# Kernel optimization log

Hardware: AMD Instinct MI355X
Metric: run time of the kernel (lower is better)

## Reference

```python
import jax, jax.numpy as jnp
import numpy as np

N, IN_DIM, HID, HEADS, OUT = 4096, 512, 256, 2, 40
LN_EPS = 1e-5


def setup_inputs() -> dict:
    key = jax.random.key(0)
    ks = jax.random.split(key, 12)
    s_in = 1.0 / np.sqrt(IN_DIM)
    s_o = 1.0 / np.sqrt(2 * HID)
    adj = jax.random.randint(ks[0], (HEADS, N, N), 0, 2).astype(jnp.float32)
    h = jax.random.normal(ks[1], (N, IN_DIM), dtype=jnp.float32)
    Wq = jax.random.uniform(ks[2], (HEADS, IN_DIM, HID), minval=-s_in, maxval=s_in)
    bq = jax.random.uniform(ks[3], (HEADS, HID), minval=-s_in, maxval=s_in)
    Wk = jax.random.uniform(ks[4], (HEADS, IN_DIM, HID), minval=-s_in, maxval=s_in)
    bk = jax.random.uniform(ks[5], (HEADS, HID), minval=-s_in, maxval=s_in)
    Wv = jax.random.uniform(ks[6], (HEADS, IN_DIM, HID), minval=-s_in, maxval=s_in)
    bv = jax.random.uniform(ks[7], (HEADS, HID), minval=-s_in, maxval=s_in)
    Wo = jax.random.uniform(ks[8], (2 * HID, IN_DIM), minval=-s_o, maxval=s_o)
    bo = jax.random.uniform(ks[9], (IN_DIM,), minval=-s_o, maxval=s_o)
    gamma = jnp.ones((IN_DIM,), jnp.float32)
    beta = jnp.zeros((IN_DIM,), jnp.float32)
    Wp = jax.random.uniform(ks[10], (IN_DIM, OUT), minval=-s_in, maxval=s_in)
    bp = jax.random.uniform(ks[11], (OUT,), minval=-s_in, maxval=s_in)
    return dict(adj=adj, h=h, Wq=Wq, bq=bq, Wk=Wk, bk=bk, Wv=Wv, bv=bv,
                Wo=Wo, bo=bo, gamma=gamma, beta=beta, Wp=Wp, bp=bp)


def reference(adj, h, Wq, bq, Wk, bk, Wv, bv, Wo, bo, gamma, beta, Wp, bp):
    # Per-head projections, vectorized over the head axis. [H, N, D]
    Q = jnp.einsum('ni,hid->hnd', h, Wq) + bq[:, None, :]
    K = jnp.einsum('ni,hid->hnd', h, Wk) + bk[:, None, :]
    V = jnp.einsum('ni,hid->hnd', h, Wv) + bv[:, None, :]
    # Dense QK^T, elementwise-multiplied (not -inf masked) by per-head adjacency.
    scores = jnp.einsum('hnd,hmd->hnm', Q, K) * adj          # [H, N, N]
    attn = jax.nn.softmax(scores, axis=-1)
    X = jnp.einsum('hnm,hmd->hnd', attn, V)                  # [H, N, D]
    # cat([X0, X1], dim=1) -> [N, H*D]
    X_final = jnp.transpose(X, (1, 0, 2)).reshape(N, HEADS * HID)
    z = X_final @ Wo + bo                                    # [N, IN_DIM]
    mu = jnp.mean(z, axis=-1, keepdims=True)
    var = jnp.var(z, axis=-1, keepdims=True)
    M = (z - mu) * jax.lax.rsqrt(var + LN_EPS) * gamma + beta
    return jax.nn.softmax(M @ Wp + bp, axis=1)               # [N, OUT]
```

## Files before the change

kernel.cpp:

```cpp
#include <hip/hip_runtime.h>
#include <hip/hip_bf16.h>

#define N_TOK 4096
#define D_IN  512
#define D_HID 256
#define N_OUT 40

typedef _Float16 half8 __attribute__((ext_vector_type(8)));
typedef _Float16 half4 __attribute__((ext_vector_type(4)));
typedef float    f32x4 __attribute__((ext_vector_type(4)));

__device__ __forceinline__ void async_copy16(const _Float16* g, _Float16* l) {
  __builtin_amdgcn_global_load_lds(
      (const __attribute__((address_space(1))) unsigned int*)(g),
      (__attribute__((address_space(3))) unsigned int*)(l), 16, 0, 0);
}

__device__ __forceinline__ void transpose_tile(const float* __restrict__ src, int in_ncols,
                                               _Float16* __restrict__ dst, int out_ncols,
                                               int i0, int d0, float* lds )
{
  int tid = threadIdx.x;
  int l15 = tid & 15, l4 = tid >> 4;
#pragma unroll
  for (int p = 0; p < 4; p++) {
    int ii = p * 16 + l4;
    float4 x = *(const float4*)(src + (size_t)(i0 + ii) * in_ncols + d0 + l15 * 4);
    lds[(l15 * 4 + 0) * 65 + ii] = x.x;
    lds[(l15 * 4 + 1) * 65 + ii] = x.y;
    lds[(l15 * 4 + 2) * 65 + ii] = x.z;
    lds[(l15 * 4 + 3) * 65 + ii] = x.w;
  }
  __syncthreads();
  int dd = tid >> 2, chunk = tid & 3;
  half8 o0, o1;
#pragma unroll
  for (int j = 0; j < 8; j++) o0[j] = (_Float16)lds[dd * 65 + chunk * 16 + j];
#pragma unroll
  for (int j = 0; j < 8; j++) o1[j] = (_Float16)lds[dd * 65 + chunk * 16 + 8 + j];
  *(half8*)(dst + (size_t)(d0 + dd) * out_ncols + i0 + chunk * 16) = o0;
  *(half8*)(dst + (size_t)(d0 + dd) * out_ncols + i0 + chunk * 16 + 8) = o1;
}

__global__ void prep_kernel(const float* __restrict__ h, const float* __restrict__ Wq,
                            const float* __restrict__ Wk, const float* __restrict__ Wv,
                            const float* __restrict__ Wo, const float* __restrict__ Wp,
                            _Float16* __restrict__ h16, _Float16* __restrict__ Wqt,
                            _Float16* __restrict__ Wkt, _Float16* __restrict__ Wvt,
                            _Float16* __restrict__ Wot, _Float16* __restrict__ Wpt)
{
  __shared__ float lds[64 * 65];
  int b = blockIdx.x, tid = threadIdx.x;
  if (b < 1024) {
    int base = b * 2048 + tid * 8;
    float4 x0 = *(const float4*)(h + base);
    float4 x1 = *(const float4*)(h + base + 4);
    half8 o;
    o[0]=(_Float16)x0.x; o[1]=(_Float16)x0.y; o[2]=(_Float16)x0.z; o[3]=(_Float16)x0.w;
    o[4]=(_Float16)x1.x; o[5]=(_Float16)x1.y; o[6]=(_Float16)x1.z; o[7]=(_Float16)x1.w;
    *(half8*)(h16 + base) = o;
  } else if (b < 1216) {
    int t = b - 1024;
    int mat = t >> 5;
    int m = mat >> 1, head = mat & 1;
    const float* W = (m==0 ? Wq : (m==1 ? Wk : Wv)) + head * (D_IN * D_HID);
    _Float16* Wt   = (m==0 ? Wqt : (m==1 ? Wkt : Wvt)) + head * (D_IN * D_HID);
    int tt = t & 31;
    int i0 = (tt >> 2) * 64, d0 = (tt & 3) * 64;
    transpose_tile(W, D_HID, Wt, D_IN, i0, d0, lds);
  } else if (b < 1280) {
    int t = b - 1216;
    int i0 = (t >> 3) * 64, d0 = (t & 7) * 64;
    transpose_tile(Wo, D_IN, Wot, D_IN, i0, d0, lds);
  } else {
    int blk = b - 1280;
    int idx = blk * 1024 + tid * 4;
    int j = idx >> 9, i = idx & 511;
    half4 o;
#pragma unroll
    for (int u = 0; u < 4; u++)
      o[u] = (j < N_OUT) ? (_Float16)Wp[(i + u) * N_OUT + j] : (_Float16)0.f;
    *(half4*)(Wpt + j * D_IN + i) = o;
  }
}

__global__ __launch_bounds__(256, 2) void proj_kernel(
    const _Float16* __restrict__ h16, const _Float16* __restrict__ W6 ,
    const _Float16* __restrict__ Wvt,
    const float* __restrict__ bq, const float* __restrict__ bk,
    const float* __restrict__ bv,
    _Float16* __restrict__ Q16, _Float16* __restrict__ K16,
    _Float16* __restrict__ VT16)
{
  __shared__ __align__(16) _Float16 Atile[128 * 64];
  __shared__ __align__(16) _Float16 Btile[128 * 64];

  int b = blockIdx.x;
  int tid = threadIdx.x, w = tid >> 6, lane = tid & 63, quad = lane >> 4, cL = lane & 15;
  int wr = w >> 1, wc = w & 1;

  const _Float16 *Asrc, *Bsrc;
  int isV;
  int m0 = 0, n0 = 0, head = 0, mh = 0;
  if (b < 256) {
    isV = 0;
    m0 = (b >> 3) * 128;
    int ct = b & 7;
    mh = ct >> 1;
    n0 = (ct & 1) * 128;
    Asrc = h16 + (size_t)m0 * D_IN;
    Bsrc = W6 + (size_t)(ct * 128) * D_IN;
  } else {
    isV = 1;
    int t = b - 256;
    head = t >> 6;
    int tt = t & 63;
    m0 = (tt >> 5) * 128;
    n0 = (tt & 31) * 128;
    Asrc = Wvt + (size_t)head * (D_HID * D_IN) + (size_t)m0 * D_IN;
    Bsrc = h16 + (size_t)n0 * D_IN;
  }

  const f32x4 z4 = {0.f, 0.f, 0.f, 0.f};
  f32x4 acc[4][4];
#pragma unroll
  for (int i = 0; i < 4; i++)
#pragma unroll
    for (int j = 0; j < 4; j++) acc[i][j] = z4;

  int r8 = lane >> 3, chs = (lane & 7) ^ r8;

  for (int kc = 0; kc < 8; kc++) {
    __syncthreads();
#pragma unroll
    for (int g = 0; g < 4; g++) {
      int row = (w * 4 + g) * 8 + r8;
      async_copy16(Asrc + (size_t)row * D_IN + kc * 64 + chs * 8, Atile + (w * 4 + g) * 512);
      async_copy16(Bsrc + (size_t)row * D_IN + kc * 64 + chs * 8, Btile + (w * 4 + g) * 512);
    }
    __syncthreads();
#pragma unroll
    for (int kk = 0; kk < 2; kk++) {
      int ch = ((kk * 4 + quad) ^ (cL & 7)) * 8;
      half8 a[4], bf[4];
#pragma unroll
      for (int mt = 0; mt < 4; mt++)
        a[mt] = *(const half8*)(Atile + (wr * 64 + mt * 16 + cL) * 64 + ch);
#pragma unroll
      for (int nt = 0; nt < 4; nt++)
        bf[nt] = *(const half8*)(Btile + (wc * 64 + nt * 16 + cL) * 64 + ch);
#pragma unroll
      for (int mt = 0; mt < 4; mt++)
#pragma unroll
        for (int nt = 0; nt < 4; nt++)
          acc[mt][nt] = __builtin_amdgcn_mfma_f32_16x16x32_f16(a[mt], bf[nt], acc[mt][nt], 0, 0, 0);
    }
  }

  if (!isV) {
    _Float16* Out = (mh < 2 ? Q16 + (size_t)mh * (N_TOK * D_HID)
                            : K16 + (size_t)(mh - 2) * (N_TOK * D_HID));
    const float* bias = (mh < 2 ? bq + mh * D_HID : bk + (mh - 2) * D_HID);
#pragma unroll
    for (int mt = 0; mt < 4; mt++) {
      int row = m0 + wr * 64 + mt * 16 + quad * 4;
#pragma unroll
      for (int nt = 0; nt < 4; nt++) {
        int colg = n0 + wc * 64 + nt * 16 + cL;
        float bb = bias[colg];
#pragma unroll
        for (int reg = 0; reg < 4; reg++)
          Out[(size_t)(row + reg) * D_HID + colg] = (_Float16)(acc[mt][nt][reg] + bb);
      }
    }
  } else {
    _Float16* VTh = VT16 + (size_t)head * (N_TOK * D_HID);
    const float* bvh = bv + head * D_HID;
#pragma unroll
    for (int mt = 0; mt < 4; mt++) {
      int d0r = m0 + wr * 64 + mt * 16 + quad * 4;
      float bvv[4];
#pragma unroll
      for (int reg = 0; reg < 4; reg++) bvv[reg] = bvh[d0r + reg];
#pragma unroll
      for (int nt = 0; nt < 4; nt++) {
        int tok = n0 + wc * 64 + nt * 16 + cL;
#pragma unroll
        for (int reg = 0; reg < 4; reg++)
          VTh[(size_t)(d0r + reg) * N_TOK + tok] = (_Float16)(acc[mt][nt][reg] + bvv[reg]);
      }
    }
  }
}

__global__ __launch_bounds__(256, 2) void attn_kernel(
    const float* __restrict__ adj, const _Float16* __restrict__ Q16,
    const _Float16* __restrict__ K16, const _Float16* __restrict__ VT16,
    _Float16* __restrict__ Opart, float* __restrict__ Mpart, float* __restrict__ Lpart)
{
  __shared__ __align__(16) _Float16 Ktile[64 * 256];
  __shared__ __align__(16) _Float16 VTtile[256 * 64];
  __shared__ __align__(16) _Float16 Pbuf[4 * 16 * 72];

  int b = blockIdx.x;
  int head = (b >> 2) & 1;
  int gs = b & 3;
  int q0 = (b >> 3) * 64;

  int tid = threadIdx.x;
  int w = tid >> 6, lane = tid & 63, quad = lane >> 4, cL = lane & 15;

  const _Float16* Qh = Q16 + head * (N_TOK * D_HID);
  const _Float16* Kh = K16 + head * (N_TOK * D_HID);
  const _Float16* Vh = VT16 + head * (N_TOK * D_HID);
  const float* adjh = adj + (size_t)head * N_TOK * N_TOK;

  int qrow = q0 + w * 16;
  int nstart = gs * 1024;
  const f32x4 z4 = {0.f, 0.f, 0.f, 0.f};

  half8 qf[8];
#pragma unroll
  for (int t = 0; t < 8; t++)
    qf[t] = *(const half8*)(Qh + (qrow + cL) * D_HID + t * 32 + quad * 8);

  f32x4 acc[16];
#pragma unroll
  for (int i = 0; i < 16; i++) acc[i] = z4;
  float m_i[4] = {-1e30f, -1e30f, -1e30f, -1e30f};
  float l_i[4] = {0.f, 0.f, 0.f, 0.f};

  _Float16* pb = Pbuf + w * (16 * 72);

  const float* adjR[4];
#pragma unroll
  for (int reg = 0; reg < 4; reg++)
    adjR[reg] = adjh + (size_t)(qrow + quad * 4 + reg) * N_TOK + nstart + cL;

  int l5 = lane >> 5, l31 = lane & 31;
  int l3 = lane >> 3, l7 = lane & 7;

  for (int it = 0; it < 16; ++it) {
    int n0 = nstart + it * 64;

    __syncthreads();

#pragma unroll
    for (int i = 0; i < 8; i++) {
      int g = w * 8 + i;
      int rK = 2 * g + l5;
      int cK = l31 ^ (rK & 7);
      async_copy16(Kh + (size_t)(n0 + rK) * D_HID + cK * 8, Ktile + g * 512);
      int rV = g * 8 + l3;
      int cV = l7 ^ (rV & 7);
      async_copy16(Vh + (size_t)rV * N_TOK + n0 + cV * 8, VTtile + g * 512);
    }
    float av[4][4];
#pragma unroll
    for (int reg = 0; reg < 4; reg++)
#pragma unroll
      for (int ct = 0; ct < 4; ct++)
        av[reg][ct] = __builtin_nontemporal_load(adjR[reg] + it * 64 + ct * 16);

    __syncthreads();

    f32x4 s[4];
#pragma unroll
    for (int ct = 0; ct < 4; ct++) s[ct] = z4;
#pragma unroll
    for (int t = 0; t < 8; t++) {
#pragma unroll
      for (int ct = 0; ct < 4; ct++) {
        int rK = ct * 16 + cL;
        int ck = (t * 4 + quad) ^ (rK & 7);
        half8 kf = *(const half8*)(Ktile + rK * 256 + ck * 8);
        s[ct] = __builtin_amdgcn_mfma_f32_16x16x32_f16(qf[t], kf, s[ct], 0, 0, 0);
      }
    }

    float alpha[4];
#pragma unroll
    for (int reg = 0; reg < 4; reg++) {
#pragma unroll
      for (int ct = 0; ct < 4; ct++) s[ct][reg] *= av[reg][ct];
      float mx = fmaxf(fmaxf(s[0][reg], s[1][reg]), fmaxf(s[2][reg], s[3][reg]));
#pragma unroll
      for (int msk = 1; msk < 16; msk <<= 1) mx = fmaxf(mx, __shfl_xor(mx, msk, 16));
      float mnew = fmaxf(m_i[reg], mx);
      alpha[reg] = __expf(m_i[reg] - mnew);
      m_i[reg] = mnew;
      float rs = 0.f;
#pragma unroll
      for (int ct = 0; ct < 4; ct++) {
        float p = __expf(s[ct][reg] - mnew);
        s[ct][reg] = p;
        rs += p;
      }
#pragma unroll
      for (int msk = 1; msk < 16; msk <<= 1) rs += __shfl_xor(rs, msk, 16);
      l_i[reg] = l_i[reg] * alpha[reg] + rs;
    }

#pragma unroll
    for (int reg = 0; reg < 4; reg++)
#pragma unroll
      for (int ct = 0; ct < 4; ct++)
        pb[(quad * 4 + reg) * 72 + ct * 16 + cL] = (_Float16)s[ct][reg];

#pragma unroll
    for (int dt = 0; dt < 16; dt++)
#pragma unroll
      for (int reg = 0; reg < 4; reg++)
        acc[dt][reg] *= alpha[reg];

    half8 pf0 = *(const half8*)(pb + cL * 72 + quad * 8);
    half8 pf1 = *(const half8*)(pb + cL * 72 + 32 + quad * 8);
#pragma unroll
    for (int dt = 0; dt < 16; dt++) {
      int rV = dt * 16 + cL;
      int c0 = (quad) ^ (rV & 7);
      int c1 = (4 + quad) ^ (rV & 7);
      half8 v0 = *(const half8*)(VTtile + rV * 64 + c0 * 8);
      half8 v1 = *(const half8*)(VTtile + rV * 64 + c1 * 8);
      acc[dt] = __builtin_amdgcn_mfma_f32_16x16x32_f16(pf0, v0, acc[dt], 0, 0, 0);
      acc[dt] = __builtin_amdgcn_mfma_f32_16x16x32_f16(pf1, v1, acc[dt], 0, 0, 0);
    }
  }

  int prow = (head * 4 + gs) * N_TOK + qrow + quad * 4;
#pragma unroll
  for (int reg = 0; reg < 4; reg++) {
    int row = prow + reg;
#pragma unroll
    for (int dt = 0; dt < 16; dt++)
      Opart[(size_t)row * D_HID + dt * 16 + cL] = (_Float16)acc[dt][reg];
    if (cL == 0) { Mpart[row] = m_i[reg]; Lpart[row] = l_i[reg]; }
  }
}

__global__ void merge_kernel(const _Float16* __restrict__ Opart,
                             const float* __restrict__ Mpart,
                             const float* __restrict__ Lpart,
                             _Float16* __restrict__ Xf)
{
  int t = blockIdx.x * 256 + threadIdx.x;
  int dg = (t & 63) << 2;
  int n = (t >> 6) & (N_TOK - 1);
  int head = t >> 18;
  int idx[4];
  float m[4], l[4];
  float mm = -1e30f;
#pragma unroll
  for (int s = 0; s < 4; s++) {
    idx[s] = (head * 4 + s) * N_TOK + n;
    m[s] = Mpart[idx[s]];
    l[s] = Lpart[idx[s]];
    mm = fmaxf(mm, m[s]);
  }
  float f[4], L = 0.f;
#pragma unroll
  for (int s = 0; s < 4; s++) { f[s] = __expf(m[s] - mm); L += f[s] * l[s]; }
  float rl = 1.0f / L;
  float o[4] = {0.f, 0.f, 0.f, 0.f};
#pragma unroll
  for (int s = 0; s < 4; s++) {
    half4 os = *(const half4*)(Opart + (size_t)idx[s] * D_HID + dg);
#pragma unroll
    for (int u = 0; u < 4; u++) o[u] += (float)os[u] * f[s];
  }
  half4 res;
#pragma unroll
  for (int u = 0; u < 4; u++) res[u] = (_Float16)(o[u] * rl);
  *(half4*)(Xf + (size_t)n * D_IN + head * D_HID + dg) = res;
}

__global__ __launch_bounds__(256, 1) void final_kernel(
    const _Float16* __restrict__ Xf, const _Float16* __restrict__ Wot,
    const _Float16* __restrict__ Wpt, const float* __restrict__ bo,
    const float* __restrict__ gamma, const float* __restrict__ beta,
    const float* __restrict__ bp, float* __restrict__ out)
{
  __shared__ __align__(16) _Float16 Btile[512 * 64];
  __shared__ __align__(16) _Float16 Mlds[16 * 520];
  __shared__ float outs[16 * 48];
  __shared__ float lnsum[4][16], lnsq[4][16];
  __shared__ float smx[16], srl[16];

  int rowbase = blockIdx.x * 16;
  int tid = threadIdx.x, w = tid >> 6, lane = tid & 63, quad = lane >> 4, cL = lane & 15;
  const f32x4 z4 = {0.f, 0.f, 0.f, 0.f};

  half8 af[16];
#pragma unroll
  for (int t = 0; t < 16; t++)
    af[t] = *(const half8*)(Xf + (rowbase + cL) * D_IN + t * 32 + quad * 8);

  f32x4 acc[8];
#pragma unroll
  for (int i = 0; i < 8; i++) acc[i] = z4;

  int r8 = lane >> 3, chs = (lane & 7) ^ r8;

  for (int kc = 0; kc < 8; kc++) {
    __syncthreads();
#pragma unroll
    for (int g = 0; g < 16; g++) {
      int row = (w * 16 + g) * 8 + r8;
      async_copy16(Wot + (size_t)row * D_IN + kc * 64 + chs * 8, Btile + (w * 16 + g) * 512);
    }
    __syncthreads();
#pragma unroll
    for (int kk = 0; kk < 2; kk++) {
      int ch = ((kk * 4 + quad) ^ (cL & 7)) * 8;
      half8 a = af[kc * 2 + kk];
      half8 bf[8];
#pragma unroll
      for (int nt = 0; nt < 8; nt++)
        bf[nt] = *(const half8*)(Btile + (w * 128 + nt * 16 + cL) * 64 + ch);
#pragma unroll
      for (int nt = 0; nt < 8; nt++)
        acc[nt] = __builtin_amdgcn_mfma_f32_16x16x32_f16(a, bf[nt], acc[nt], 0, 0, 0);
    }
  }

  float sum[4] = {0, 0, 0, 0}, sq[4] = {0, 0, 0, 0};
#pragma unroll
  for (int nt = 0; nt < 8; nt++) {
    int col = w * 128 + nt * 16 + cL;
    float bb = bo[col];
#pragma unroll
    for (int reg = 0; reg < 4; reg++) {
      float z = acc[nt][reg] + bb;
      acc[nt][reg] = z;
      sum[reg] += z;
      sq[reg] += z * z;
    }
  }
#pragma unroll
  for (int reg = 0; reg < 4; reg++) {
#pragma unroll
    for (int msk = 1; msk < 16; msk <<= 1) {
      sum[reg] += __shfl_xor(sum[reg], msk, 16);
      sq[reg]  += __shfl_xor(sq[reg], msk, 16);
    }
  }
  if (cL == 0) {
#pragma unroll
    for (int reg = 0; reg < 4; reg++) {
      lnsum[w][quad * 4 + reg] = sum[reg];
      lnsq[w][quad * 4 + reg]  = sq[reg];
    }
  }
  __syncthreads();
  float mean[4], rstd[4];
#pragma unroll
  for (int reg = 0; reg < 4; reg++) {
    int row = quad * 4 + reg;
    float s  = lnsum[0][row] + lnsum[1][row] + lnsum[2][row] + lnsum[3][row];
    float s2 = lnsq[0][row]  + lnsq[1][row]  + lnsq[2][row]  + lnsq[3][row];
    float mu = s * (1.0f / 512.0f);
    float var = s2 * (1.0f / 512.0f) - mu * mu;
    mean[reg] = mu;
    rstd[reg] = rsqrtf(var + 1e-5f);
  }
#pragma unroll
  for (int nt = 0; nt < 8; nt++) {
    int col = w * 128 + nt * 16 + cL;
    float g = gamma[col], be = beta[col];
#pragma unroll
    for (int reg = 0; reg < 4; reg++) {
      float mval = (acc[nt][reg] - mean[reg]) * rstd[reg] * g + be;
      Mlds[(quad * 4 + reg) * 520 + col] = (_Float16)mval;
    }
  }
  __syncthreads();
  if (w < 3) {
    int jt = w;
    f32x4 a2 = z4;
#pragma unroll
    for (int t = 0; t < 16; t++) {
      half8 am = *(const half8*)(Mlds + cL * 520 + t * 32 + quad * 8);
      half8 bm = *(const half8*)(Wpt + (jt * 16 + cL) * D_IN + t * 32 + quad * 8);
      a2 = __builtin_amdgcn_mfma_f32_16x16x32_f16(am, bm, a2, 0, 0, 0);
    }
    int col = jt * 16 + cL;
    float bpv = (col < N_OUT) ? bp[col] : 0.0f;
#pragma unroll
    for (int reg = 0; reg < 4; reg++)
      outs[(quad * 4 + reg) * 48 + col] = a2[reg] + bpv;
  }
  __syncthreads();
  if (tid < 16) {
    int row = tid;
    float mx = -1e30f;
    for (int j = 0; j < N_OUT; j++) mx = fmaxf(mx, outs[row * 48 + j]);
    float ssum = 0.f;
    for (int j = 0; j < N_OUT; j++) ssum += __expf(outs[row * 48 + j] - mx);
    smx[row] = mx;
    srl[row] = 1.0f / ssum;
  }
  __syncthreads();
#pragma unroll
  for (int i = 0; i < 3; i++) {
    int lin = tid + 256 * i;
    if (lin < 16 * N_OUT) {
      int row = lin / N_OUT, col = lin % N_OUT;
      out[(size_t)(rowbase + row) * N_OUT + col] =
          __expf(outs[row * 48 + col] - smx[row]) * srl[row];
    }
  }
}

#define OFF_WOT   0u
#define OFF_WPT   524288u
#define OFF_Q16   573440u
#define OFF_K16   4767744u
#define OFF_VT16  8962048u
#define OFF_MP    13156352u
#define OFF_LP    13287424u
#define OFF_XF    13418496u
#define OFF_OP    17612800u
#define OFF_H16   17612800u
#define OFF_WQT   21807104u
#define OFF_WKT   22331392u
#define OFF_WVT   22855680u

extern "C" void kernel_launch(void* const* d_in, const int* in_sizes, int n_in,
                              void* d_out, int out_size, void* d_ws, size_t ws_size,
                              hipStream_t stream)
{
  const float* adj   = (const float*)d_in[0];
  const float* h     = (const float*)d_in[1];
  const float* Wq    = (const float*)d_in[2];
  const float* bq    = (const float*)d_in[3];
  const float* Wk    = (const float*)d_in[4];
  const float* bk    = (const float*)d_in[5];
  const float* Wv    = (const float*)d_in[6];
  const float* bv    = (const float*)d_in[7];
  const float* Wo    = (const float*)d_in[8];
  const float* bo    = (const float*)d_in[9];
  const float* gamma = (const float*)d_in[10];
  const float* beta  = (const float*)d_in[11];
  const float* Wp    = (const float*)d_in[12];
  const float* bp    = (const float*)d_in[13];
  float* out = (float*)d_out;
  char* ws = (char*)d_ws;

  _Float16* h16   = (_Float16*)(ws + OFF_H16);
  _Float16* Wqt   = (_Float16*)(ws + OFF_WQT);
  _Float16* Wkt   = (_Float16*)(ws + OFF_WKT);
  _Float16* Wvt   = (_Float16*)(ws + OFF_WVT);
  _Float16* Wot   = (_Float16*)(ws + OFF_WOT);
  _Float16* Wpt   = (_Float16*)(ws + OFF_WPT);
  _Float16* Q16   = (_Float16*)(ws + OFF_Q16);
  _Float16* K16   = (_Float16*)(ws + OFF_K16);
  _Float16* VT16  = (_Float16*)(ws + OFF_VT16);
  _Float16* Opart = (_Float16*)(ws + OFF_OP);
  float*    Mpart = (float*)(ws + OFF_MP);
  float*    Lpart = (float*)(ws + OFF_LP);
  _Float16* Xf    = (_Float16*)(ws + OFF_XF);

  prep_kernel<<<1304, 256, 0, stream>>>(h, Wq, Wk, Wv, Wo, Wp,
                                        h16, Wqt, Wkt, Wvt, Wot, Wpt);
  proj_kernel<<<384, 256, 0, stream>>>(h16, Wqt, Wvt, bq, bk, bv,
                                       Q16, K16, VT16);
  attn_kernel<<<512, 256, 0, stream>>>(adj, Q16, K16, VT16, Opart, Mpart, Lpart);
  merge_kernel<<<2048, 256, 0, stream>>>(Opart, Mpart, Lpart, Xf);
  final_kernel<<<256, 256, 0, stream>>>(Xf, Wot, Wpt, bo, gamma, beta, bp, out);
}
```

Measured before the change: 297.9 us.

## Fuse all stages into one cooperative persistent kernel with grid syncs

```diff
diff --git a/kernel.cpp b/kernel.cpp
--- a/kernel.cpp
+++ b/kernel.cpp
@@ -1,5 +1,5 @@
 #include <hip/hip_runtime.h>
-#include <hip/hip_bf16.h>
+#include <hip/hip_cooperative_groups.h>
 
 #define N_TOK 4096
 #define D_IN  512
@@ -16,500 +16,11 @@
       (__attribute__((address_space(3))) unsigned int*)(l), 16, 0, 0);
 }
 
-__device__ __forceinline__ void transpose_tile(const float* __restrict__ src, int in_ncols,
-                                               _Float16* __restrict__ dst, int out_ncols,
-                                               int i0, int d0, float* lds )
-{
-  int tid = threadIdx.x;
-  int l15 = tid & 15, l4 = tid >> 4;
-#pragma unroll
-  for (int p = 0; p < 4; p++) {
-    int ii = p * 16 + l4;
-    float4 x = *(const float4*)(src + (size_t)(i0 + ii) * in_ncols + d0 + l15 * 4);
-    lds[(l15 * 4 + 0) * 65 + ii] = x.x;
-    lds[(l15 * 4 + 1) * 65 + ii] = x.y;
-    lds[(l15 * 4 + 2) * 65 + ii] = x.z;
-    lds[(l15 * 4 + 3) * 65 + ii] = x.w;
-  }
-  __syncthreads();
-  int dd = tid >> 2, chunk = tid & 3;
-  half8 o0, o1;
-#pragma unroll
-  for (int j = 0; j < 8; j++) o0[j] = (_Float16)lds[dd * 65 + chunk * 16 + j];
-#pragma unroll
-  for (int j = 0; j < 8; j++) o1[j] = (_Float16)lds[dd * 65 + chunk * 16 + 8 + j];
-  *(half8*)(dst + (size_t)(d0 + dd) * out_ncols + i0 + chunk * 16) = o0;
-  *(half8*)(dst + (size_t)(d0 + dd) * out_ncols + i0 + chunk * 16 + 8) = o1;
-}
-
-__global__ void prep_kernel(const float* __restrict__ h, const float* __restrict__ Wq,
-                            const float* __restrict__ Wk, const float* __restrict__ Wv,
-                            const float* __restrict__ Wo, const float* __restrict__ Wp,
-                            _Float16* __restrict__ h16, _Float16* __restrict__ Wqt,
-                            _Float16* __restrict__ Wkt, _Float16* __restrict__ Wvt,
-                            _Float16* __restrict__ Wot, _Float16* __restrict__ Wpt)
-{
-  __shared__ float lds[64 * 65];
-  int b = blockIdx.x, tid = threadIdx.x;
-  if (b < 1024) {
-    int base = b * 2048 + tid * 8;
-    float4 x0 = *(const float4*)(h + base);
-    float4 x1 = *(const float4*)(h + base + 4);
-    half8 o;
-    o[0]=(_Float16)x0.x; o[1]=(_Float16)x0.y; o[2]=(_Float16)x0.z; o[3]=(_Float16)x0.w;
-    o[4]=(_Float16)x1.x; o[5]=(_Float16)x1.y; o[6]=(_Float16)x1.z; o[7]=(_Float16)x1.w;
-    *(half8*)(h16 + base) = o;
-  } else if (b < 1216) {
-    int t = b - 1024;
-    int mat = t >> 5;
-    int m = mat >> 1, head = mat & 1;
-    const float* W = (m==0 ? Wq : (m==1 ? Wk : Wv)) + head * (D_IN * D_HID);
-    _Float16* Wt   = (m==0 ? Wqt : (m==1 ? Wkt : Wvt)) + head * (D_IN * D_HID);
-    int tt = t & 31;
-    int i0 = (tt >> 2) * 64, d0 = (tt & 3) * 64;
-    transpose_tile(W, D_HID, Wt, D_IN, i0, d0, lds);
-  } else if (b < 1280) {
-    int t = b - 1216;
-    int i0 = (t >> 3) * 64, d0 = (t & 7) * 64;
-    transpose_tile(Wo, D_IN, Wot, D_IN, i0, d0, lds);
-  } else {
-    int blk = b - 1280;
-    int idx = blk * 1024 + tid * 4;
-    int j = idx >> 9, i = idx & 511;
-    half4 o;
-#pragma unroll
-    for (int u = 0; u < 4; u++)
-      o[u] = (j < N_OUT) ? (_Float16)Wp[(i + u) * N_OUT + j] : (_Float16)0.f;
-    *(half4*)(Wpt + j * D_IN + i) = o;
-  }
-}
-
-__global__ __launch_bounds__(256, 2) void proj_kernel(
-    const _Float16* __restrict__ h16, const _Float16* __restrict__ W6 ,
-    const _Float16* __restrict__ Wvt,
-    const float* __restrict__ bq, const float* __restrict__ bk,
-    const float* __restrict__ bv,
-    _Float16* __restrict__ Q16, _Float16* __restrict__ K16,
-    _Float16* __restrict__ VT16)
-{
-  __shared__ __align__(16) _Float16 Atile[128 * 64];
-  __shared__ __align__(16) _Float16 Btile[128 * 64];
-
-  int b = blockIdx.x;
-  int tid = threadIdx.x, w = tid >> 6, lane = tid & 63, quad = lane >> 4, cL = lane & 15;
-  int wr = w >> 1, wc = w & 1;
-
-  const _Float16 *Asrc, *Bsrc;
-  int isV;
-  int m0 = 0, n0 = 0, head = 0, mh = 0;
-  if (b < 256) {
-    isV = 0;
-    m0 = (b >> 3) * 128;
-    int ct = b & 7;
-    mh = ct >> 1;
-    n0 = (ct & 1) * 128;
-    Asrc = h16 + (size_t)m0 * D_IN;
-    Bsrc = W6 + (size_t)(ct * 128) * D_IN;
-  } else {
-    isV = 1;
-    int t = b - 256;
-    head = t >> 6;
-    int tt = t & 63;
-    m0 = (tt >> 5) * 128;
-    n0 = (tt & 31) * 128;
-    Asrc = Wvt + (size_t)head * (D_HID * D_IN) + (size_t)m0 * D_IN;
-    Bsrc = h16 + (size_t)n0 * D_IN;
-  }
-
-  const f32x4 z4 = {0.f, 0.f, 0.f, 0.f};
-  f32x4 acc[4][4];
-#pragma unroll
-  for (int i = 0; i < 4; i++)
-#pragma unroll
-    for (int j = 0; j < 4; j++) acc[i][j] = z4;
-
-  int r8 = lane >> 3, chs = (lane & 7) ^ r8;
-
-  for (int kc = 0; kc < 8; kc++) {
-    __syncthreads();
-#pragma unroll
-    for (int g = 0; g < 4; g++) {
-      int row = (w * 4 + g) * 8 + r8;
-      async_copy16(Asrc + (size_t)row * D_IN + kc * 64 + chs * 8, Atile + (w * 4 + g) * 512);
-      async_copy16(Bsrc + (size_t)row * D_IN + kc * 64 + chs * 8, Btile + (w * 4 + g) * 512);
-    }
-    __syncthreads();
-#pragma unroll
-    for (int kk = 0; kk < 2; kk++) {
-      int ch = ((kk * 4 + quad) ^ (cL & 7)) * 8;
-      half8 a[4], bf[4];
-#pragma unroll
-      for (int mt = 0; mt < 4; mt++)
-        a[mt] = *(const half8*)(Atile + (wr * 64 + mt * 16 + cL) * 64 + ch);
-#pragma unroll
-      for (int nt = 0; nt < 4; nt++)
-        bf[nt] = *(const half8*)(Btile + (wc * 64 + nt * 16 + cL) * 64 + ch);
-#pragma unroll
-      for (int mt = 0; mt < 4; mt++)
-#pragma unroll
-        for (int nt = 0; nt < 4; nt++)
-          acc[mt][nt] = __builtin_amdgcn_mfma_f32_16x16x32_f16(a[mt], bf[nt], acc[mt][nt], 0, 0, 0);
-    }
-  }
-
-  if (!isV) {
-    _Float16* Out = (mh < 2 ? Q16 + (size_t)mh * (N_TOK * D_HID)
-                            : K16 + (size_t)(mh - 2) * (N_TOK * D_HID));
-    const float* bias = (mh < 2 ? bq + mh * D_HID : bk + (mh - 2) * D_HID);
-#pragma unroll
-    for (int mt = 0; mt < 4; mt++) {
-      int row = m0 + wr * 64 + mt * 16 + quad * 4;
-#pragma unroll
-      for (int nt = 0; nt < 4; nt++) {
-        int colg = n0 + wc * 64 + nt * 16 + cL;
-        float bb = bias[colg];
-#pragma unroll
-        for (int reg = 0; reg < 4; reg++)
-          Out[(size_t)(row + reg) * D_HID + colg] = (_Float16)(acc[mt][nt][reg] + bb);
-      }
-    }
-  } else {
-    _Float16* VTh = VT16 + (size_t)head * (N_TOK * D_HID);
-    const float* bvh = bv + head * D_HID;
-#pragma unroll
-    for (int mt = 0; mt < 4; mt++) {
-      int d0r = m0 + wr * 64 + mt * 16 + quad * 4;
-      float bvv[4];
-#pragma unroll
-      for (int reg = 0; reg < 4; reg++) bvv[reg] = bvh[d0r + reg];
-#pragma unroll
-      for (int nt = 0; nt < 4; nt++) {
-        int tok = n0 + wc * 64 + nt * 16 + cL;
-#pragma unroll
-        for (int reg = 0; reg < 4; reg++)
-          VTh[(size_t)(d0r + reg) * N_TOK + tok] = (_Float16)(acc[mt][nt][reg] + bvv[reg]);
-      }
-    }
-  }
-}
-
-__global__ __launch_bounds__(256, 2) void attn_kernel(
-    const float* __restrict__ adj, const _Float16* __restrict__ Q16,
-    const _Float16* __restrict__ K16, const _Float16* __restrict__ VT16,
-    _Float16* __restrict__ Opart, float* __restrict__ Mpart, float* __restrict__ Lpart)
-{
-  __shared__ __align__(16) _Float16 Ktile[64 * 256];
-  __shared__ __align__(16) _Float16 VTtile[256 * 64];
-  __shared__ __align__(16) _Float16 Pbuf[4 * 16 * 72];
-
-  int b = blockIdx.x;
-  int head = (b >> 2) & 1;
-  int gs = b & 3;
-  int q0 = (b >> 3) * 64;
-
-  int tid = threadIdx.x;
-  int w = tid >> 6, lane = tid & 63, quad = lane >> 4, cL = lane & 15;
-
-  const _Float16* Qh = Q16 + head * (N_TOK * D_HID);
-  const _Float16* Kh = K16 + head * (N_TOK * D_HID);
-  const _Float16* Vh = VT16 + head * (N_TOK * D_HID);
-  const float* adjh = adj + (size_t)head * N_TOK * N_TOK;
-
-  int qrow = q0 + w * 16;
-  int nstart = gs * 1024;
-  const f32x4 z4 = {0.f, 0.f, 0.f, 0.f};
-
-  half8 qf[8];
-#pragma unroll
-  for (int t = 0; t < 8; t++)
-    qf[t] = *(const half8*)(Qh + (qrow + cL) * D_HID + t * 32 + quad * 8);
-
-  f32x4 acc[16];
-#pragma unroll
-  for (int i = 0; i < 16; i++) acc[i] = z4;
-  float m_i[4] = {-1e30f, -1e30f, -1e30f, -1e30f};
-  float l_i[4] = {0.f, 0.f, 0.f, 0.f};
-
-  _Float16* pb = Pbuf + w * (16 * 72);
-
-  const float* adjR[4];
-#pragma unroll
-  for (int reg = 0; reg < 4; reg++)
-    adjR[reg] = adjh + (size_t)(qrow + quad * 4 + reg) * N_TOK + nstart + cL;
-
-  int l5 = lane >> 5, l31 = lane & 31;
-  int l3 = lane >> 3, l7 = lane & 7;
-
-  for (int it = 0; it < 16; ++it) {
-    int n0 = nstart + it * 64;
-
-    __syncthreads();
-
-#pragma unroll
-    for (int i = 0; i < 8; i++) {
-      int g = w * 8 + i;
-      int rK = 2 * g + l5;
-      int cK = l31 ^ (rK & 7);
-      async_copy16(Kh + (size_t)(n0 + rK) * D_HID + cK * 8, Ktile + g * 512);
-      int rV = g * 8 + l3;
-      int cV = l7 ^ (rV & 7);
-      async_copy16(Vh + (size_t)rV * N_TOK + n0 + cV * 8, VTtile + g * 512);
-    }
-    float av[4][4];
-#pragma unroll
-    for (int reg = 0; reg < 4; reg++)
-#pragma unroll
-      for (int ct = 0; ct < 4; ct++)
-        av[reg][ct] = __builtin_nontemporal_load(adjR[reg] + it * 64 + ct * 16);
-
-    __syncthreads();
-
-    f32x4 s[4];
-#pragma unroll
-    for (int ct = 0; ct < 4; ct++) s[ct] = z4;
-#pragma unroll
-    for (int t = 0; t < 8; t++) {
-#pragma unroll
-      for (int ct = 0; ct < 4; ct++) {
-        int rK = ct * 16 + cL;
-        int ck = (t * 4 + quad) ^ (rK & 7);
-        half8 kf = *(const half8*)(Ktile + rK * 256 + ck * 8);
-        s[ct] = __builtin_amdgcn_mfma_f32_16x16x32_f16(qf[t], kf, s[ct], 0, 0, 0);
-      }
-    }
-
-    float alpha[4];
-#pragma unroll
-    for (int reg = 0; reg < 4; reg++) {
-#pragma unroll
-      for (int ct = 0; ct < 4; ct++) s[ct][reg] *= av[reg][ct];
-      float mx = fmaxf(fmaxf(s[0][reg], s[1][reg]), fmaxf(s[2][reg], s[3][reg]));
-#pragma unroll
-      for (int msk = 1; msk < 16; msk <<= 1) mx = fmaxf(mx, __shfl_xor(mx, msk, 16));
-      float mnew = fmaxf(m_i[reg], mx);
-      alpha[reg] = __expf(m_i[reg] - mnew);
-      m_i[reg] = mnew;
-      float rs = 0.f;
-#pragma unroll
-      for (int ct = 0; ct < 4; ct++) {
-        float p = __expf(s[ct][reg] - mnew);
-        s[ct][reg] = p;
-        rs += p;
-      }
-#pragma unroll
-      for (int msk = 1; msk < 16; msk <<= 1) rs += __shfl_xor(rs, msk, 16);
-      l_i[reg] = l_i[reg] * alpha[reg] + rs;
-    }
-
-#pragma unroll
-    for (int reg = 0; reg < 4; reg++)
-#pragma unroll
-      for (int ct = 0; ct < 4; ct++)
-        pb[(quad * 4 + reg) * 72 + ct * 16 + cL] = (_Float16)s[ct][reg];
-
-#pragma unroll
-    for (int dt = 0; dt < 16; dt++)
-#pragma unroll
-      for (int reg = 0; reg < 4; reg++)
-        acc[dt][reg] *= alpha[reg];
-
-    half8 pf0 = *(const half8*)(pb + cL * 72 + quad * 8);
-    half8 pf1 = *(const half8*)(pb + cL * 72 + 32 + quad * 8);
-#pragma unroll
-    for (int dt = 0; dt < 16; dt++) {
-      int rV = dt * 16 + cL;
-      int c0 = (quad) ^ (rV & 7);
-      int c1 = (4 + quad) ^ (rV & 7);
-      half8 v0 = *(const half8*)(VTtile + rV * 64 + c0 * 8);
-      half8 v1 = *(const half8*)(VTtile + rV * 64 + c1 * 8);
-      acc[dt] = __builtin_amdgcn_mfma_f32_16x16x32_f16(pf0, v0, acc[dt], 0, 0, 0);
-      acc[dt] = __builtin_amdgcn_mfma_f32_16x16x32_f16(pf1, v1, acc[dt], 0, 0, 0);
-    }
-  }
-
-  int prow = (head * 4 + gs) * N_TOK + qrow + quad * 4;
-#pragma unroll
-  for (int reg = 0; reg < 4; reg++) {
-    int row = prow + reg;
-#pragma unroll
-    for (int dt = 0; dt < 16; dt++)
-      Opart[(size_t)row * D_HID + dt * 16 + cL] = (_Float16)acc[dt][reg];
-    if (cL == 0) { Mpart[row] = m_i[reg]; Lpart[row] = l_i[reg]; }
-  }
-}
-
-__global__ void merge_kernel(const _Float16* __restrict__ Opart,
-                             const float* __restrict__ Mpart,
-                             const float* __restrict__ Lpart,
-                             _Float16* __restrict__ Xf)
-{
-  int t = blockIdx.x * 256 + threadIdx.x;
-  int dg = (t & 63) << 2;
-  int n = (t >> 6) & (N_TOK - 1);
-  int head = t >> 18;
-  int idx[4];
-  float m[4], l[4];
-  float mm = -1e30f;
-#pragma unroll
-  for (int s = 0; s < 4; s++) {
-    idx[s] = (head * 4 + s) * N_TOK + n;
-    m[s] = Mpart[idx[s]];
-    l[s] = Lpart[idx[s]];
-    mm = fmaxf(mm, m[s]);
-  }
-  float f[4], L = 0.f;
-#pragma unroll
-  for (int s = 0; s < 4; s++) { f[s] = __expf(m[s] - mm); L += f[s] * l[s]; }
-  float rl = 1.0f / L;
-  float o[4] = {0.f, 0.f, 0.f, 0.f};
-#pragma unroll
-  for (int s = 0; s < 4; s++) {
-    half4 os = *(const half4*)(Opart + (size_t)idx[s] * D_HID + dg);
-#pragma unroll
-    for (int u = 0; u < 4; u++) o[u] += (float)os[u] * f[s];
-  }
-  half4 res;
-#pragma unroll
-  for (int u = 0; u < 4; u++) res[u] = (_Float16)(o[u] * rl);
-  *(half4*)(Xf + (size_t)n * D_IN + head * D_HID + dg) = res;
-}
-
-__global__ __launch_bounds__(256, 1) void final_kernel(
-    const _Float16* __restrict__ Xf, const _Float16* __restrict__ Wot,
-    const _Float16* __restrict__ Wpt, const float* __restrict__ bo,
-    const float* __restrict__ gamma, const float* __restrict__ beta,
-    const float* __restrict__ bp, float* __restrict__ out)
-{
-  __shared__ __align__(16) _Float16 Btile[512 * 64];
-  __shared__ __align__(16) _Float16 Mlds[16 * 520];
-  __shared__ float outs[16 * 48];
-  __shared__ float lnsum[4][16], lnsq[4][16];
-  __shared__ float smx[16], srl[16];
-
-  int rowbase = blockIdx.x * 16;
-  int tid = threadIdx.x, w = tid >> 6, lane = tid & 63, quad = lane >> 4, cL = lane & 15;
-  const f32x4 z4 = {0.f, 0.f, 0.f, 0.f};
-
-  half8 af[16];
-#pragma unroll
-  for (int t = 0; t < 16; t++)
-    af[t] = *(const half8*)(Xf + (rowbase + cL) * D_IN + t * 32 + quad * 8);
-
-  f32x4 acc[8];
-#pragma unroll
-  for (int i = 0; i < 8; i++) acc[i] = z4;
-
-  int r8 = lane >> 3, chs = (lane & 7) ^ r8;
-
-  for (int kc = 0; kc < 8; kc++) {
-    __syncthreads();
-#pragma unroll
-    for (int g = 0; g < 16; g++) {
-      int row = (w * 16 + g) * 8 + r8;
-      async_copy16(Wot + (size_t)row * D_IN + kc * 64 + chs * 8, Btile + (w * 16 + g) * 512);
-    }
-    __syncthreads();
-#pragma unroll
-    for (int kk = 0; kk < 2; kk++) {
-      int ch = ((kk * 4 + quad) ^ (cL & 7)) * 8;
-      half8 a = af[kc * 2 + kk];
-      half8 bf[8];
-#pragma unroll
-      for (int nt = 0; nt < 8; nt++)
-        bf[nt] = *(const half8*)(Btile + (w * 128 + nt * 16 + cL) * 64 + ch);
-#pragma unroll
-      for (int nt = 0; nt < 8; nt++)
-        acc[nt] = __builtin_amdgcn_mfma_f32_16x16x32_f16(a, bf[nt], acc[nt], 0, 0, 0);
-    }
-  }
-
-  float sum[4] = {0, 0, 0, 0}, sq[4] = {0, 0, 0, 0};
-#pragma unroll
-  for (int nt = 0; nt < 8; nt++) {
-    int col = w * 128 + nt * 16 + cL;
-    float bb = bo[col];
-#pragma unroll
-    for (int reg = 0; reg < 4; reg++) {
-      float z = acc[nt][reg] + bb;
-      acc[nt][reg] = z;
-      sum[reg] += z;
-      sq[reg] += z * z;
-    }
-  }
-#pragma unroll
-  for (int reg = 0; reg < 4; reg++) {
-#pragma unroll
-    for (int msk = 1; msk < 16; msk <<= 1) {
-      sum[reg] += __shfl_xor(sum[reg], msk, 16);
-      sq[reg]  += __shfl_xor(sq[reg], msk, 16);
-    }
-  }
-  if (cL == 0) {
-#pragma unroll
-    for (int reg = 0; reg < 4; reg++) {
-      lnsum[w][quad * 4 + reg] = sum[reg];
-      lnsq[w][quad * 4 + reg]  = sq[reg];
-    }
-  }
-  __syncthreads();
-  float mean[4], rstd[4];
-#pragma unroll
-  for (int reg = 0; reg < 4; reg++) {
-    int row = quad * 4 + reg;
-    float s  = lnsum[0][row] + lnsum[1][row] + lnsum[2][row] + lnsum[3][row];
-    float s2 = lnsq[0][row]  + lnsq[1][row]  + lnsq[2][row]  + lnsq[3][row];
-    float mu = s * (1.0f / 512.0f);
-    float var = s2 * (1.0f / 512.0f) - mu * mu;
-    mean[reg] = mu;
-    rstd[reg] = rsqrtf(var + 1e-5f);
-  }
-#pragma unroll
-  for (int nt = 0; nt < 8; nt++) {
-    int col = w * 128 + nt * 16 + cL;
-    float g = gamma[col], be = beta[col];
-#pragma unroll
-    for (int reg = 0; reg < 4; reg++) {
-      float mval = (acc[nt][reg] - mean[reg]) * rstd[reg] * g + be;
-      Mlds[(quad * 4 + reg) * 520 + col] = (_Float16)mval;
-    }
-  }
-  __syncthreads();
-  if (w < 3) {
-    int jt = w;
-    f32x4 a2 = z4;
-#pragma unroll
-    for (int t = 0; t < 16; t++) {
-      half8 am = *(const half8*)(Mlds + cL * 520 + t * 32 + quad * 8);
-      half8 bm = *(const half8*)(Wpt + (jt * 16 + cL) * D_IN + t * 32 + quad * 8);
-      a2 = __builtin_amdgcn_mfma_f32_16x16x32_f16(am, bm, a2, 0, 0, 0);
-    }
-    int col = jt * 16 + cL;
-    float bpv = (col < N_OUT) ? bp[col] : 0.0f;
-#pragma unroll
-    for (int reg = 0; reg < 4; reg++)
-      outs[(quad * 4 + reg) * 48 + col] = a2[reg] + bpv;
-  }
-  __syncthreads();
-  if (tid < 16) {
-    int row = tid;
-    float mx = -1e30f;
-    for (int j = 0; j < N_OUT; j++) mx = fmaxf(mx, outs[row * 48 + j]);
-    float ssum = 0.f;
-    for (int j = 0; j < N_OUT; j++) ssum += __expf(outs[row * 48 + j] - mx);
-    smx[row] = mx;
-    srl[row] = 1.0f / ssum;
-  }
-  __syncthreads();
-#pragma unroll
-  for (int i = 0; i < 3; i++) {
-    int lin = tid + 256 * i;
-    if (lin < 16 * N_OUT) {
-      int row = lin / N_OUT, col = lin % N_OUT;
-      out[(size_t)(rowbase + row) * N_OUT + col] =
-          __expf(outs[row * 48 + col] - smx[row]) * srl[row];
-    }
-  }
-}
+struct Params {
+  const float *adj, *h, *Wq, *bq, *Wk, *bk, *Wv, *bv, *Wo, *bo, *gamma, *beta, *Wp, *bp;
+  float* out;
+  char* ws;
+};
 
 #define OFF_WOT   0u
 #define OFF_WPT   524288u
@@ -518,53 +29,528 @@
 #define OFF_VT16  8962048u
 #define OFF_MP    13156352u
 #define OFF_LP    13287424u
-#define OFF_XF    13418496u
 #define OFF_OP    17612800u
 #define OFF_H16   17612800u
 #define OFF_WQT   21807104u
 #define OFF_WKT   22331392u
 #define OFF_WVT   22855680u
 
+__global__ __launch_bounds__(256, 2) void fused_kernel(Params P, int phase)
+{
+  __shared__ __align__(16) char smem[74752];
+  const int bid = blockIdx.x, tid = threadIdx.x;
+  const int w = tid >> 6, lane = tid & 63, quad = lane >> 4, cL = lane & 15;
+  const f32x4 z4 = {0.f, 0.f, 0.f, 0.f};
+
+  char* ws = P.ws;
+  _Float16* Wot  = (_Float16*)(ws + OFF_WOT);
+  _Float16* Wpt  = (_Float16*)(ws + OFF_WPT);
+  _Float16* Q16  = (_Float16*)(ws + OFF_Q16);
+  _Float16* K16  = (_Float16*)(ws + OFF_K16);
+  _Float16* VT16 = (_Float16*)(ws + OFF_VT16);
+  float*    Mp   = (float*)   (ws + OFF_MP);
+  float*    Lp   = (float*)   (ws + OFF_LP);
+  _Float16* Op   = (_Float16*)(ws + OFF_OP);
+  _Float16* h16  = (_Float16*)(ws + OFF_H16);
+  _Float16* Wqt  = (_Float16*)(ws + OFF_WQT);
+  _Float16* Wkt  = (_Float16*)(ws + OFF_WKT);
+  _Float16* Wvt  = (_Float16*)(ws + OFF_WVT);
+
+  if (phase == -1 || phase == 0) {
+    float* lds = (float*)smem;
+    for (int job = bid; job < 1304; job += 512) {
+      if (job < 1024) {
+        int base = job * 2048 + tid * 8;
+        float4 x0 = *(const float4*)(P.h + base);
+        float4 x1 = *(const float4*)(P.h + base + 4);
+        half8 o;
+        o[0]=(_Float16)x0.x; o[1]=(_Float16)x0.y; o[2]=(_Float16)x0.z; o[3]=(_Float16)x0.w;
+        o[4]=(_Float16)x1.x; o[5]=(_Float16)x1.y; o[6]=(_Float16)x1.z; o[7]=(_Float16)x1.w;
+        *(half8*)(h16 + base) = o;
+      } else if (job < 1280) {
+        const float* src; _Float16* dst; int in_nc, i0, d0;
+        if (job < 1216) {
+          int t = job - 1024;
+          int mat = t >> 5;
+          int m = mat >> 1, head = mat & 1;
+          src = (m==0 ? P.Wq : (m==1 ? P.Wk : P.Wv)) + head * (D_IN * D_HID);
+          dst = (m==0 ? Wqt : (m==1 ? Wkt : Wvt)) + head * (D_IN * D_HID);
+          in_nc = D_HID;
+          int tt = t & 31;
+          i0 = (tt >> 2) * 64; d0 = (tt & 3) * 64;
+        } else {
+          int t = job - 1216;
+          src = P.Wo; dst = Wot; in_nc = D_IN;
+          i0 = (t >> 3) * 64; d0 = (t & 7) * 64;
+        }
+        int l15 = tid & 15, l4 = tid >> 4;
+#pragma unroll
+        for (int p = 0; p < 4; p++) {
+          int ii = p * 16 + l4;
+          float4 x = *(const float4*)(src + (size_t)(i0 + ii) * in_nc + d0 + l15 * 4);
+          lds[(l15 * 4 + 0) * 65 + ii] = x.x;
+          lds[(l15 * 4 + 1) * 65 + ii] = x.y;
+          lds[(l15 * 4 + 2) * 65 + ii] = x.z;
+          lds[(l15 * 4 + 3) * 65 + ii] = x.w;
+        }
+        __syncthreads();
+        int dd = tid >> 2, chunk = tid & 3;
+        half8 o0, o1;
+#pragma unroll
+        for (int j = 0; j < 8; j++) o0[j] = (_Float16)lds[dd * 65 + chunk * 16 + j];
+#pragma unroll
+        for (int j = 0; j < 8; j++) o1[j] = (_Float16)lds[dd * 65 + chunk * 16 + 8 + j];
+        *(half8*)(dst + (size_t)(d0 + dd) * D_IN + i0 + chunk * 16) = o0;
+        *(half8*)(dst + (size_t)(d0 + dd) * D_IN + i0 + chunk * 16 + 8) = o1;
+      } else {
+        int blk = job - 1280;
+        int idx = blk * 1024 + tid * 4;
+        int j = idx >> 9, i = idx & 511;
+        half4 o;
+#pragma unroll
+        for (int u = 0; u < 4; u++)
+          o[u] = (j < N_OUT) ? (_Float16)P.Wp[(i + u) * N_OUT + j] : (_Float16)0.f;
+        *(half4*)(Wpt + j * D_IN + i) = o;
+      }
+      __syncthreads();
+    }
+  }
+  if (phase < 0) { __threadfence(); cooperative_groups::this_grid().sync(); }
+
+  if ((phase == -1 || phase == 1) && bid < 384) {
+    _Float16* Atile = (_Float16*)smem;
+    _Float16* Btile = (_Float16*)(smem + 16384);
+    int wr = w >> 1, wc = w & 1;
+    const _Float16 *Asrc, *Bsrc;
+    int isV = 0, m0, n0, head = 0, mh = 0;
+    if (bid < 256) {
+      m0 = (bid >> 3) * 128;
+      int ct = bid & 7;
+      mh = ct >> 1;
+      n0 = (ct & 1) * 128;
+      Asrc = h16 + (size_t)m0 * D_IN;
+      Bsrc = Wqt + (size_t)(ct * 128) * D_IN;
+    } else {
+      isV = 1;
+      int t = bid - 256;
+      head = t >> 6;
+      int tt = t & 63;
+      m0 = (tt >> 5) * 128;
+      n0 = (tt & 31) * 128;
+      Asrc = Wvt + (size_t)head * (D_HID * D_IN) + (size_t)m0 * D_IN;
+      Bsrc = h16 + (size_t)n0 * D_IN;
+    }
+    f32x4 acc[4][4];
+#pragma unroll
+    for (int i = 0; i < 4; i++)
+#pragma unroll
+      for (int j = 0; j < 4; j++) acc[i][j] = z4;
+    int r8 = lane >> 3, chs = (lane & 7) ^ r8;
+    for (int kc = 0; kc < 8; kc++) {
+      __syncthreads();
+#pragma unroll
+      for (int g = 0; g < 4; g++) {
+        int row = (w * 4 + g) * 8 + r8;
+        async_copy16(Asrc + (size_t)row * D_IN + kc * 64 + chs * 8, Atile + (w * 4 + g) * 512);
+        async_copy16(Bsrc + (size_t)row * D_IN + kc * 64 + chs * 8, Btile + (w * 4 + g) * 512);
+      }
+      __syncthreads();
+#pragma unroll
+      for (int kk = 0; kk < 2; kk++) {
+        int ch = ((kk * 4 + quad) ^ (cL & 7)) * 8;
+        half8 a[4], bf[4];
+#pragma unroll
+        for (int mt = 0; mt < 4; mt++)
+          a[mt] = *(const half8*)(Atile + (wr * 64 + mt * 16 + cL) * 64 + ch);
+#pragma unroll
+        for (int nt = 0; nt < 4; nt++)
+          bf[nt] = *(const half8*)(Btile + (wc * 64 + nt * 16 + cL) * 64 + ch);
+#pragma unroll
+        for (int mt = 0; mt < 4; mt++)
+#pragma unroll
+          for (int nt = 0; nt < 4; nt++)
+            acc[mt][nt] = __builtin_amdgcn_mfma_f32_16x16x32_f16(a[mt], bf[nt], acc[mt][nt], 0, 0, 0);
+      }
+    }
+    if (!isV) {
+      _Float16* Out = (mh < 2 ? Q16 + (size_t)mh * (N_TOK * D_HID)
+                              : K16 + (size_t)(mh - 2) * (N_TOK * D_HID));
+      const float* bias = (mh < 2 ? P.bq + mh * D_HID : P.bk + (mh - 2) * D_HID);
+#pragma unroll
+      for (int mt = 0; mt < 4; mt++) {
+        int row = m0 + wr * 64 + mt * 16 + quad * 4;
+#pragma unroll
+        for (int nt = 0; nt < 4; nt++) {
+          int colg = n0 + wc * 64 + nt * 16 + cL;
+          float bb = bias[colg];
+#pragma unroll
+          for (int reg = 0; reg < 4; reg++)
+            Out[(size_t)(row + reg) * D_HID + colg] = (_Float16)(acc[mt][nt][reg] + bb);
+        }
+      }
+    } else {
+      _Float16* VTh = VT16 + (size_t)head * (N_TOK * D_HID);
+      const float* bvh = P.bv + head * D_HID;
+#pragma unroll
+      for (int mt = 0; mt < 4; mt++) {
+        int d0r = m0 + wr * 64 + mt * 16 + quad * 4;
+        float bvv[4];
+#pragma unroll
+        for (int reg = 0; reg < 4; reg++) bvv[reg] = bvh[d0r + reg];
+#pragma unroll
+        for (int nt = 0; nt < 4; nt++) {
+          int tok = n0 + wc * 64 + nt * 16 + cL;
+#pragma unroll
+          for (int reg = 0; reg < 4; reg++)
+            VTh[(size_t)(d0r + reg) * N_TOK + tok] = (_Float16)(acc[mt][nt][reg] + bvv[reg]);
+        }
+      }
+    }
+  }
+  if (phase < 0) { __threadfence(); cooperative_groups::this_grid().sync(); }
+
+  if (phase == -1 || phase == 2) {
+    _Float16* Ktile  = (_Float16*)smem;
+    _Float16* VTtile = (_Float16*)(smem + 32768);
+    _Float16* Pbuf   = (_Float16*)(smem + 65536);
+
+    int head = (bid >> 2) & 1;
+    int gs = bid & 3;
+    int q0 = (bid >> 3) * 64;
+
+    const _Float16* Qh = Q16 + head * (N_TOK * D_HID);
+    const _Float16* Kh = K16 + head * (N_TOK * D_HID);
+    const _Float16* Vh = VT16 + head * (N_TOK * D_HID);
+    const float* adjh = P.adj + (size_t)head * N_TOK * N_TOK;
+
+    int qrow = q0 + w * 16;
+    int nstart = gs * 1024;
+
+    half8 qf[8];
+#pragma unroll
+    for (int t = 0; t < 8; t++)
+      qf[t] = *(const half8*)(Qh + (qrow + cL) * D_HID + t * 32 + quad * 8);
+
+    f32x4 acc[16];
+#pragma unroll
+    for (int i = 0; i < 16; i++) acc[i] = z4;
+    float m_i[4] = {-1e30f, -1e30f, -1e30f, -1e30f};
+    float l_i[4] = {0.f, 0.f, 0.f, 0.f};
+
+    _Float16* pb = Pbuf + w * (16 * 72);
+
+    const float* adjR[4];
+#pragma unroll
+    for (int reg = 0; reg < 4; reg++)
+      adjR[reg] = adjh + (size_t)(qrow + quad * 4 + reg) * N_TOK + nstart + cL;
+
+    int l5 = lane >> 5, l31 = lane & 31;
+    int l3 = lane >> 3, l7 = lane & 7;
+
+    for (int it = 0; it < 16; ++it) {
+      int n0 = nstart + it * 64;
+
+      __syncthreads();
+
+#pragma unroll
+      for (int i = 0; i < 8; i++) {
+        int g = w * 8 + i;
+        int rK = 2 * g + l5;
+        int cK = l31 ^ (rK & 7);
+        async_copy16(Kh + (size_t)(n0 + rK) * D_HID + cK * 8, Ktile + g * 512);
+        int rV = g * 8 + l3;
+        int cV = l7 ^ (rV & 7);
+        async_copy16(Vh + (size_t)rV * N_TOK + n0 + cV * 8, VTtile + g * 512);
+      }
+      float av[4][4];
+#pragma unroll
+      for (int reg = 0; reg < 4; reg++)
+#pragma unroll
+        for (int ct = 0; ct < 4; ct++)
+          av[reg][ct] = __builtin_nontemporal_load(adjR[reg] + it * 64 + ct * 16);
+
+      __syncthreads();
+
+      f32x4 s[4];
+#pragma unroll
+      for (int ct = 0; ct < 4; ct++) s[ct] = z4;
+#pragma unroll
+      for (int t = 0; t < 8; t++) {
+#pragma unroll
+        for (int ct = 0; ct < 4; ct++) {
+          int rK = ct * 16 + cL;
+          int ck = (t * 4 + quad) ^ (rK & 7);
+          half8 kf = *(const half8*)(Ktile + rK * 256 + ck * 8);
+          s[ct] = __builtin_amdgcn_mfma_f32_16x16x32_f16(qf[t], kf, s[ct], 0, 0, 0);
+        }
+      }
+
+      float alpha[4];
+#pragma unroll
+      for (int reg = 0; reg < 4; reg++) {
+#pragma unroll
+        for (int ct = 0; ct < 4; ct++) s[ct][reg] *= av[reg][ct];
+        float mx = fmaxf(fmaxf(s[0][reg], s[1][reg]), fmaxf(s[2][reg], s[3][reg]));
+#pragma unroll
+        for (int msk = 1; msk < 16; msk <<= 1) mx = fmaxf(mx, __shfl_xor(mx, msk, 16));
+        float mnew = fmaxf(m_i[reg], mx);
+        alpha[reg] = __expf(m_i[reg] - mnew);
+        m_i[reg] = mnew;
+        float rs = 0.f;
+#pragma unroll
+        for (int ct = 0; ct < 4; ct++) {
+          float p = __expf(s[ct][reg] - mnew);
+          s[ct][reg] = p;
+          rs += p;
+        }
+#pragma unroll
+        for (int msk = 1; msk < 16; msk <<= 1) rs += __shfl_xor(rs, msk, 16);
+        l_i[reg] = l_i[reg] * alpha[reg] + rs;
+      }
+
+#pragma unroll
+      for (int reg = 0; reg < 4; reg++)
+#pragma unroll
+        for (int ct = 0; ct < 4; ct++)
+          pb[(quad * 4 + reg) * 72 + ct * 16 + cL] = (_Float16)s[ct][reg];
+
+#pragma unroll
+      for (int dt = 0; dt < 16; dt++)
+#pragma unroll
+        for (int reg = 0; reg < 4; reg++)
+          acc[dt][reg] *= alpha[reg];
+
+      half8 pf0 = *(const half8*)(pb + cL * 72 + quad * 8);
+      half8 pf1 = *(const half8*)(pb + cL * 72 + 32 + quad * 8);
+#pragma unroll
+      for (int dt = 0; dt < 16; dt++) {
+        int rV = dt * 16 + cL;
+        int c0 = (quad) ^ (rV & 7);
+        int c1 = (4 + quad) ^ (rV & 7);
+        half8 v0 = *(const half8*)(VTtile + rV * 64 + c0 * 8);
+        half8 v1 = *(const half8*)(VTtile + rV * 64 + c1 * 8);
+        acc[dt] = __builtin_amdgcn_mfma_f32_16x16x32_f16(pf0, v0, acc[dt], 0, 0, 0);
+        acc[dt] = __builtin_amdgcn_mfma_f32_16x16x32_f16(pf1, v1, acc[dt], 0, 0, 0);
+      }
+    }
+
+    int prow = (head * 4 + gs) * N_TOK + qrow + quad * 4;
+#pragma unroll
+    for (int reg = 0; reg < 4; reg++) {
+      int row = prow + reg;
+#pragma unroll
+      for (int dt = 0; dt < 16; dt++)
+        Op[(size_t)row * D_HID + dt * 16 + cL] = (_Float16)acc[dt][reg];
+      if (cL == 0) { Mp[row] = m_i[reg]; Lp[row] = l_i[reg]; }
+    }
+  }
+  if (phase < 0) { __threadfence(); cooperative_groups::this_grid().sync(); }
+
+  if ((phase == -1 || phase == 3) && bid < 256) {
+    _Float16* Btile = (_Float16*)smem;
+    _Float16* Mlds  = (_Float16*)smem;
+    float* outs  = (float*)(smem + 66560);
+    float* lnsum = (float*)(smem + 69632);
+    float* lnsq  = (float*)(smem + 69888);
+    float* smx   = (float*)(smem + 70144);
+    float* srl   = (float*)(smem + 70208);
+
+    int rowbase = bid * 16;
+    int zrow = rowbase + cL;
+
+    float wgt[2][4];
+#pragma unroll
+    for (int hh = 0; hh < 2; hh++) {
+      float m[4], l[4], mm = -1e30f;
+#pragma unroll
+      for (int s = 0; s < 4; s++) {
+        int idx = (hh * 4 + s) * N_TOK + zrow;
+        m[s] = Mp[idx]; l[s] = Lp[idx];
+        mm = fmaxf(mm, m[s]);
+      }
+      float f[4], denom = 0.f;
+#pragma unroll
+      for (int s = 0; s < 4; s++) { f[s] = __expf(m[s] - mm); denom += f[s] * l[s]; }
+      float inv = 1.0f / fmaxf(denom, 1e-30f);
+#pragma unroll
+      for (int s = 0; s < 4; s++) wgt[hh][s] = f[s] * inv;
+    }
+    half8 af[16];
+#pragma unroll
+    for (int t = 0; t < 16; t++) {
+      int hh = t >> 3;
+      int dcol = (t & 7) * 32 + quad * 8;
+      float a8[8] = {0, 0, 0, 0, 0, 0, 0, 0};
+#pragma unroll
+      for (int s = 0; s < 4; s++) {
+        half8 o = *(const half8*)(Op + ((size_t)((hh * 4 + s) * N_TOK + zrow)) * D_HID + dcol);
+        float wv = wgt[hh][s];
+#pragma unroll
+        for (int j = 0; j < 8; j++) a8[j] += wv * (float)o[j];
+      }
+      half8 v;
+#pragma unroll
+      for (int j = 0; j < 8; j++) v[j] = (_Float16)a8[j];
+      af[t] = v;
+    }
+
+    f32x4 acc[8];
+#pragma unroll
+    for (int i = 0; i < 8; i++) acc[i] = z4;
+    int r8 = lane >> 3, chs = (lane & 7) ^ r8;
+    for (int kc = 0; kc < 8; kc++) {
+      __syncthreads();
+#pragma unroll
+      for (int g = 0; g < 16; g++) {
+        int row = (w * 16 + g) * 8 + r8;
+        async_copy16(Wot + (size_t)row * D_IN + kc * 64 + chs * 8, Btile + (w * 16 + g) * 512);
+      }
+      __syncthreads();
+#pragma unroll
+      for (int kk = 0; kk < 2; kk++) {
+        int ch = ((kk * 4 + quad) ^ (cL & 7)) * 8;
+        half8 a = af[kc * 2 + kk];
+        half8 bf[8];
+#pragma unroll
+        for (int nt = 0; nt < 8; nt++)
+          bf[nt] = *(const half8*)(Btile + (w * 128 + nt * 16 + cL) * 64 + ch);
+#pragma unroll
+        for (int nt = 0; nt < 8; nt++)
+          acc[nt] = __builtin_amdgcn_mfma_f32_16x16x32_f16(a, bf[nt], acc[nt], 0, 0, 0);
+      }
+    }
+
+    float sum[4] = {0, 0, 0, 0}, sq[4] = {0, 0, 0, 0};
+#pragma unroll
+    for (int nt = 0; nt < 8; nt++) {
+      int col = w * 128 + nt * 16 + cL;
+      float bb = P.bo[col];
+#pragma unroll
+      for (int reg = 0; reg < 4; reg++) {
+        float z = acc[nt][reg] + bb;
+        acc[nt][reg] = z;
+        sum[reg] += z;
+        sq[reg] += z * z;
+      }
+    }
+#pragma unroll
+    for (int reg = 0; reg < 4; reg++) {
+#pragma unroll
+      for (int msk = 1; msk < 16; msk <<= 1) {
+        sum[reg] += __shfl_xor(sum[reg], msk, 16);
+        sq[reg]  += __shfl_xor(sq[reg], msk, 16);
+      }
+    }
+    if (cL == 0) {
+#pragma unroll
+      for (int reg = 0; reg < 4; reg++) {
+        lnsum[w * 16 + quad * 4 + reg] = sum[reg];
+        lnsq[w * 16 + quad * 4 + reg]  = sq[reg];
+      }
+    }
+    __syncthreads();
+    float mean[4], rstd[4];
+#pragma unroll
+    for (int reg = 0; reg < 4; reg++) {
+      int row = quad * 4 + reg;
+      float ssm = lnsum[row] + lnsum[16 + row] + lnsum[32 + row] + lnsum[48 + row];
+      float s2  = lnsq[row]  + lnsq[16 + row]  + lnsq[32 + row]  + lnsq[48 + row];
+      float mu = ssm * (1.0f / 512.0f);
+      float var = s2 * (1.0f / 512.0f) - mu * mu;
+      mean[reg] = mu;
+      rstd[reg] = rsqrtf(var + 1e-5f);
+    }
+#pragma unroll
+    for (int nt = 0; nt < 8; nt++) {
+      int col = w * 128 + nt * 16 + cL;
+      float g = P.gamma[col], be = P.beta[col];
+#pragma unroll
+      for (int reg = 0; reg < 4; reg++) {
+        float mval = (acc[nt][reg] - mean[reg]) * rstd[reg] * g + be;
+        Mlds[(quad * 4 + reg) * 520 + col] = (_Float16)mval;
+      }
+    }
+    __syncthreads();
+    if (w < 3) {
+      f32x4 a2 = z4;
+#pragma unroll
+      for (int t = 0; t < 16; t++) {
+        half8 am = *(const half8*)(Mlds + cL * 520 + t * 32 + quad * 8);
+        half8 bm = *(const half8*)(Wpt + (w * 16 + cL) * D_IN + t * 32 + quad * 8);
+        a2 = __builtin_amdgcn_mfma_f32_16x16x32_f16(am, bm, a2, 0, 0, 0);
+      }
+      int col = w * 16 + cL;
+      float bpv = (col < N_OUT) ? P.bp[col] : 0.0f;
+#pragma unroll
+      for (int reg = 0; reg < 4; reg++)
+        outs[(quad * 4 + reg) * 48 + col] = a2[reg] + bpv;
+    }
+    __syncthreads();
+    if (tid < 16) {
+      int row = tid;
+      float mx = -1e30f;
+      for (int j = 0; j < N_OUT; j++) mx = fmaxf(mx, outs[row * 48 + j]);
+      float ssum = 0.f;
+      for (int j = 0; j < N_OUT; j++) ssum += __expf(outs[row * 48 + j] - mx);
+      smx[row] = mx;
+      srl[row] = 1.0f / ssum;
+    }
+    __syncthreads();
+#pragma unroll
+    for (int i = 0; i < 3; i++) {
+      int lin = tid + 256 * i;
+      if (lin < 16 * N_OUT) {
+        int row = lin / N_OUT, col = lin % N_OUT;
+        P.out[(size_t)(rowbase + row) * N_OUT + col] =
+            __expf(outs[row * 48 + col] - smx[row]) * srl[row];
+      }
+    }
+  }
+}
+
 extern "C" void kernel_launch(void* const* d_in, const int* in_sizes, int n_in,
                               void* d_out, int out_size, void* d_ws, size_t ws_size,
                               hipStream_t stream)
 {
-  const float* adj   = (const float*)d_in[0];
-  const float* h     = (const float*)d_in[1];
-  const float* Wq    = (const float*)d_in[2];
-  const float* bq    = (const float*)d_in[3];
-  const float* Wk    = (const float*)d_in[4];
-  const float* bk    = (const float*)d_in[5];
-  const float* Wv    = (const float*)d_in[6];
-  const float* bv    = (const float*)d_in[7];
-  const float* Wo    = (const float*)d_in[8];
-  const float* bo    = (const float*)d_in[9];
-  const float* gamma = (const float*)d_in[10];
-  const float* beta  = (const float*)d_in[11];
-  const float* Wp    = (const float*)d_in[12];
-  const float* bp    = (const float*)d_in[13];
-  float* out = (float*)d_out;
-  char* ws = (char*)d_ws;
-
-  _Float16* h16   = (_Float16*)(ws + OFF_H16);
-  _Float16* Wqt   = (_Float16*)(ws + OFF_WQT);
-  _Float16* Wkt   = (_Float16*)(ws + OFF_WKT);
-  _Float16* Wvt   = (_Float16*)(ws + OFF_WVT);
-  _Float16* Wot   = (_Float16*)(ws + OFF_WOT);
-  _Float16* Wpt   = (_Float16*)(ws + OFF_WPT);
-  _Float16* Q16   = (_Float16*)(ws + OFF_Q16);
-  _Float16* K16   = (_Float16*)(ws + OFF_K16);
-  _Float16* VT16  = (_Float16*)(ws + OFF_VT16);
-  _Float16* Opart = (_Float16*)(ws + OFF_OP);
-  float*    Mpart = (float*)(ws + OFF_MP);
-  float*    Lpart = (float*)(ws + OFF_LP);
-  _Float16* Xf    = (_Float16*)(ws + OFF_XF);
-
-  prep_kernel<<<1304, 256, 0, stream>>>(h, Wq, Wk, Wv, Wo, Wp,
-                                        h16, Wqt, Wkt, Wvt, Wot, Wpt);
-  proj_kernel<<<384, 256, 0, stream>>>(h16, Wqt, Wvt, bq, bk, bv,
-                                       Q16, K16, VT16);
-  attn_kernel<<<512, 256, 0, stream>>>(adj, Q16, K16, VT16, Opart, Mpart, Lpart);
-  merge_kernel<<<2048, 256, 0, stream>>>(Opart, Mpart, Lpart, Xf);
-  final_kernel<<<256, 256, 0, stream>>>(Xf, Wot, Wpt, bo, gamma, beta, bp, out);
+  Params P;
+  P.adj   = (const float*)d_in[0];
+  P.h     = (const float*)d_in[1];
+  P.Wq    = (const float*)d_in[2];
+  P.bq    = (const float*)d_in[3];
+  P.Wk    = (const float*)d_in[4];
+  P.bk    = (const float*)d_in[5];
+  P.Wv    = (const float*)d_in[6];
+  P.bv    = (const float*)d_in[7];
+  P.Wo    = (const float*)d_in[8];
+  P.bo    = (const float*)d_in[9];
+  P.gamma = (const float*)d_in[10];
+  P.beta  = (const float*)d_in[11];
+  P.Wp    = (const float*)d_in[12];
+  P.bp    = (const float*)d_in[13];
+  P.out   = (float*)d_out;
+  P.ws    = (char*)d_ws;
+
+  bool coop_ok = false;
+  int dev = 0, attr = 0;
+  if (hipGetDevice(&dev) == hipSuccess &&
+      hipDeviceGetAttribute(&attr, hipDeviceAttributeCooperativeLaunch, dev) == hipSuccess &&
+      attr) {
+    int maxBlocks = 0;
+    if (hipOccupancyMaxActiveBlocksPerMultiprocessor(
+            &maxBlocks, (const void*)fused_kernel, 256, 0) == hipSuccess &&
+        maxBlocks >= 2) {
+      int phase = -1;
+      void* args[] = { &P, &phase };
+      hipError_t e = hipLaunchCooperativeKernel((const void*)fused_kernel,
+                                                dim3(512), dim3(256), args, 0, stream);
+      if (e == hipSuccess) coop_ok = true;
+    }
+  }
+  if (!coop_ok) {
+    (void)hipGetLastError();
+    fused_kernel<<<512, 256, 0, stream>>>(P, 0);
+    fused_kernel<<<512, 256, 0, stream>>>(P, 1);
+    fused_kernel<<<512, 256, 0, stream>>>(P, 2);
+    fused_kernel<<<512, 256, 0, stream>>>(P, 3);
+  }
 }
```

Measured after the change: 299.9 us. No clear change (+0.7%).
